# Kernel tuning notes

Hardware: AMD Instinct MI355X
Metric: run time of the kernel (lower is better)

## Reference

```python
import jax, jax.numpy as jnp
import numpy as np

E = 2048      # embedding_size
H = 16        # num_heads
D = 128       # head_dim
G = 4         # gqa_factor
KH = H // G   # kv heads
F = 8192      # up_proj_size
B, S = 2, 2048


def _layer_norm(x, g, b, eps=1e-5):
    mu = jnp.mean(x, axis=-1, keepdims=True)
    var = jnp.mean(jnp.square(x - mu), axis=-1, keepdims=True)
    return (x - mu) * jax.lax.rsqrt(var + eps) * g + b


def setup_inputs() -> dict:
    key = jax.random.key(0)
    ks = jax.random.split(key, 16)
    std = 0.02
    inp = {
        'x': jax.random.normal(ks[0], (B, S, E), dtype=jnp.float32),
        'ln1_g': jnp.ones((E,), jnp.float32),
        'ln1_b': jnp.zeros((E,), jnp.float32),
        'wq': jax.random.normal(ks[1], (E, H * D), jnp.float32) * std,
        'bq': jnp.zeros((H * D,), jnp.float32),
        'wk': jax.random.normal(ks[2], (E, KH * D), jnp.float32) * std,
        'bk': jnp.zeros((KH * D,), jnp.float32),
        'wv': jax.random.normal(ks[3], (E, KH * D), jnp.float32) * std,
        'bv': jnp.zeros((KH * D,), jnp.float32),
        'wo': jax.random.normal(ks[4], (H * D, E), jnp.float32) * std,
        'bo': jnp.zeros((E,), jnp.float32),
        'ln2_g': jnp.ones((E,), jnp.float32),
        'ln2_b': jnp.zeros((E,), jnp.float32),
        'wu': jax.random.normal(ks[5], (E, F), jnp.float32) * std,
        'bu': jnp.zeros((F,), jnp.float32),
        'wd': jax.random.normal(ks[6], (F, E), jnp.float32) * std,
        'bd': jnp.zeros((E,), jnp.float32),
    }
    return inp


def _block(x, ln1_g, ln1_b, wq, bq, wk, bk, wv, bv, wo, bo, ln2_g, ln2_b, wu, bu, wd, bd):
    b, s, e = x.shape
    # attention sub-block (use_cache=False, train_mode=False -> no dropout)
    x1 = _layer_norm(x, ln1_g, ln1_b)
    q = (x1 @ wq + bq).reshape(b, s, H, D).transpose(0, 2, 1, 3)       # (B,H,S,D)
    q = q.reshape(b, KH, G, s, D)                                       # (B,KH,G,S,D)
    k = (x1 @ wk + bk).reshape(b, s, KH, D).transpose(0, 2, 1, 3)      # (B,KH,S,D)
    v = (x1 @ wv + bv).reshape(b, s, KH, D).transpose(0, 2, 1, 3)      # (B,KH,S,D)
    scores = jnp.einsum('bkgsd,bktd->bkgst', q, k) / np.sqrt(D).astype(np.float32)
    causal = jnp.tril(jnp.ones((s, s), dtype=bool))                     # True = keep
    scores = jnp.where(causal, scores, -jnp.inf)
    att = jax.nn.softmax(scores, axis=-1)
    o = jnp.einsum('bkgst,bktd->bkgsd', att, v)                         # (B,KH,G,S,D)
    o = o.reshape(b, H, s, D).transpose(0, 2, 1, 3).reshape(b, s, H * D)
    x = x + (o @ wo + bo)
    # MLP sub-block
    x2 = _layer_norm(x, ln2_g, ln2_b)
    h = jax.nn.gelu(x2 @ wu + bu, approximate=False)
    x = x + (h @ wd + bd)
    return x


def reference(x, ln1_g, ln1_b, wq, bq, wk, bk, wv, bv, wo, bo, ln2_g, ln2_b, wu, bu, wd, bd):
    return _block(x, ln1_g, ln1_b, wq, bq, wk, bk, wv, bv, wo, bo, ln2_g, ln2_b, wu, bu, wd, bd)
```

## Files before the change

kernel.cpp:

```cpp
#include <hip/hip_runtime.h>
#include <hip/hip_bf16.h>
#include <cstdint>
#include <math.h>

typedef unsigned short u16;
using f32x4   = __attribute__((ext_vector_type(4))) float;
using short8  = __attribute__((ext_vector_type(8))) short;
using short4v = __attribute__((ext_vector_type(4))) short;

#define DEV static __device__ __forceinline__

DEV u16 f2bf(float f) {
  union { float f; unsigned u; } v; v.f = f;
  unsigned r = v.u + 0x7fffu + ((v.u >> 16) & 1u);
  return (u16)(r >> 16);
}

DEV f32x4 mfma_bf16(short8 a, short8 b, f32x4 c) {
  return __builtin_amdgcn_mfma_f32_16x16x32_bf16(a, b, c, 0, 0, 0);
}

DEV void gload16(const void* g, void* l) {
  __builtin_amdgcn_global_load_lds((const __attribute__((address_space(1))) void*)g,
                                   (__attribute__((address_space(3))) void*)l,
                                   16, 0, 0);
}

__global__ __launch_bounds__(256) void transpose_cvt(
    const float* __restrict__ in, u16* __restrict__ out, int K, int N)
{
  __shared__ float tile[32][33];
  const int n0 = blockIdx.x * 32, k0 = blockIdx.y * 32;
  const int c = threadIdx.x & 31, r = threadIdx.x >> 5;
#pragma unroll
  for (int i = 0; i < 4; i++) {
    const int row = r + i * 8;
    tile[row][c] = in[(size_t)(k0 + row) * N + n0 + c];
  }
  __syncthreads();
#pragma unroll
  for (int i = 0; i < 4; i++) {
    const int row = r + i * 8;
    out[(size_t)(n0 + row) * K + k0 + c] = f2bf(tile[c][row]);
  }
}

__global__ __launch_bounds__(256) void ln_kernel(
    const float* __restrict__ x, const float* __restrict__ g,
    const float* __restrict__ bt, u16* __restrict__ out)
{
  __shared__ float red1[4], red2[4];
  const int row = blockIdx.x;
  const int t = threadIdx.x;
  const int lane = t & 63, w = t >> 6;
  const float* xr = x + (size_t)row * 2048 + t * 8;
  float v[8];
  {
    const float4* p4 = (const float4*)xr;
    float4 a = p4[0], b = p4[1];
    v[0] = a.x; v[1] = a.y; v[2] = a.z; v[3] = a.w;
    v[4] = b.x; v[5] = b.y; v[6] = b.z; v[7] = b.w;
  }
  float s = 0.f;
#pragma unroll
  for (int j = 0; j < 8; j++) s += v[j];
#pragma unroll
  for (int m = 1; m < 64; m <<= 1) s += __shfl_xor(s, m);
  if (lane == 0) red1[w] = s;
  __syncthreads();
  const float mu = (red1[0] + red1[1] + red1[2] + red1[3]) * (1.f / 2048.f);
  float q = 0.f;
#pragma unroll
  for (int j = 0; j < 8; j++) { v[j] -= mu; q += v[j] * v[j]; }
#pragma unroll
  for (int m = 1; m < 64; m <<= 1) q += __shfl_xor(q, m);
  if (lane == 0) red2[w] = q;
  __syncthreads();
  const float rstd = rsqrtf((red2[0] + red2[1] + red2[2] + red2[3]) * (1.f / 2048.f) + 1e-5f);
  const float4* g4 = (const float4*)(g + t * 8);
  const float4* b4 = (const float4*)(bt + t * 8);
  float4 ga = g4[0], gb = g4[1], ba = b4[0], bb = b4[1];
  float gg[8] = {ga.x, ga.y, ga.z, ga.w, gb.x, gb.y, gb.z, gb.w};
  float bbv[8] = {ba.x, ba.y, ba.z, ba.w, bb.x, bb.y, bb.z, bb.w};
  short8 o;
#pragma unroll
  for (int j = 0; j < 8; j++) o[j] = (short)f2bf(v[j] * rstd * gg[j] + bbv[j]);
  *(short8*)&out[(size_t)row * 2048 + t * 8] = o;
}

template<int MODE, int N, int K>
__global__ void __launch_bounds__(256) gemm_bt(
    const u16* __restrict__ A, const u16* __restrict__ Bt,
    const float* __restrict__ bias,
    u16* __restrict__ out_bf)
{
  __shared__ u16 As[128 * 64];
  __shared__ u16 Bs[128 * 64];
  const int m0 = blockIdx.y * 128;
  const int n0 = blockIdx.x * 128;
  const int tid = threadIdx.x;
  const int lane = tid & 63, w = tid >> 6;
  const int wm = w >> 1, wn = w & 1;
  const int z = lane >> 4, l15 = lane & 15;

  f32x4 acc[4][4];
#pragma unroll
  for (int m = 0; m < 4; m++)
#pragma unroll
    for (int n = 0; n < 4; n++)
#pragma unroll
      for (int i = 0; i < 4; i++) acc[m][n][i] = 0.f;

  for (int k0 = 0; k0 < K; k0 += 64) {
#pragma unroll
    for (int j = 0; j < 4; j++) {
      const int seg = w * 4 + j;
      const int c = seg * 64 + lane;
      const int r = c >> 3;
      const int cc = (c & 7) ^ (r & 7);
      gload16(A + (size_t)(m0 + r) * K + k0 + cc * 8, &As[seg * 512]);
    }
#pragma unroll
    for (int j = 0; j < 4; j++) {
      const int seg = w * 4 + j;
      const int c = seg * 64 + lane;
      const int r = c >> 3;
      const int cc = (c & 7) ^ (r & 7);
      gload16(Bt + (size_t)(n0 + r) * K + k0 + cc * 8, &Bs[seg * 512]);
    }
    asm volatile("s_waitcnt vmcnt(0)" ::: "memory");
    __syncthreads();

#pragma unroll
    for (int kk = 0; kk < 2; kk++) {
      short8 af[4], bfr[4];
#pragma unroll
      for (int m = 0; m < 4; m++) {
        const int row = wm * 64 + m * 16 + l15;
        const int off = row * 64 + ((kk * 32 + z * 8) ^ ((row & 7) << 3));
        af[m] = *(const short8*)&As[off];
      }
#pragma unroll
      for (int n = 0; n < 4; n++) {
        const int row = wn * 64 + n * 16 + l15;
        const int off = row * 64 + ((kk * 32 + z * 8) ^ ((row & 7) << 3));
        bfr[n] = *(const short8*)&Bs[off];
      }
#pragma unroll
      for (int m = 0; m < 4; m++)
#pragma unroll
        for (int n = 0; n < 4; n++)
          acc[m][n] = mfma_bf16(af[m], bfr[n], acc[m][n]);
    }
    __syncthreads();
  }

#pragma unroll
  for (int m = 0; m < 4; m++) {
    const int row0 = m0 + wm * 64 + m * 16 + z * 4;
#pragma unroll
    for (int n = 0; n < 4; n++) {
      const int col = n0 + wn * 64 + n * 16 + l15;
      f32x4 v = acc[m][n];
      const float bb = bias[col];
      if constexpr (MODE == 1) {
#pragma unroll
        for (int i = 0; i < 4; i++)
          out_bf[(size_t)(row0 + i) * N + col] = f2bf(v[i] + bb);
      } else {
        const int bidx = row0 >> 11, sidx = row0 & 2047;
        const int kh = col >> 7, d = col & 127;
        short4v p;
#pragma unroll
        for (int i = 0; i < 4; i++) p[i] = (short)f2bf(v[i] + bb);
        *(short4v*)&out_bf[(size_t)((bidx * 4 + kh) * 128 + d) * 2048 + sidx] = p;
      }
    }
  }
}

template<int MODE, int BM, int N, int K>
__global__ void __launch_bounds__(512) gemm256(
    const u16* __restrict__ A, const u16* __restrict__ Bt,
    const float* __restrict__ bias, const float* __restrict__ resid,
    u16* __restrict__ out_bf, float* __restrict__ out_f)
{
  constexpr int BN = 256;
  constexpr int MREP = BM / 32;
  constexpr int LA = BM / 128;
  constexpr int P = K / 32;
  constexpr int NWG = (4096 / BM) * (N / BN);
  constexpr int CPX = NWG / 8;

  __shared__ u16 Al[4][BM * 32];
  __shared__ u16 Bl[4][BN * 32];

  const int bid = blockIdx.x;
  const int wg = (bid & 7) * CPX + (bid >> 3);
  const int bm = wg / (N / BN), bn = wg % (N / BN);
  const int m0 = bm * BM, n0 = bn * BN;
  const int tid = threadIdx.x, lane = tid & 63, w = tid >> 6;
  const int wm = w >> 2, wn = w & 3;
  const int z = lane >> 4, l15 = lane & 15;
  const int wmBase = wm * (BM / 2);
  const int wnBase = wn * 64;
  const int koff = (z ^ ((l15 >> 1) & 3)) * 8;
  const int col8 = ((lane & 3) ^ ((lane >> 3) & 3)) * 8;
  const int srow = lane >> 2;

  f32x4 acc[MREP][4];
#pragma unroll
  for (int m = 0; m < MREP; m++)
#pragma unroll
    for (int n = 0; n < 4; n++)
#pragma unroll
      for (int i = 0; i < 4; i++) acc[m][n][i] = 0.f;

  auto stage = [&](int g) {
    const int sl = g & 3;
    const int kc = g * 32;
#pragma unroll
    for (int j = 0; j < LA; j++) {
      const int sweep = w * LA + j;
      gload16(A + (size_t)(m0 + sweep * 16 + srow) * K + kc + col8, &Al[sl][sweep * 512]);
    }
#pragma unroll
    for (int j = 0; j < 2; j++) {
      const int sweep = w * 2 + j;
      gload16(Bt + (size_t)(n0 + sweep * 16 + srow) * K + kc + col8, &Bl[sl][sweep * 512]);
    }
  };

#define PHASE(pp, VMSTR, DOSTAGE)                                              \
  do {                                                                         \
    asm volatile("s_waitcnt " VMSTR ::: "memory");                             \
    __builtin_amdgcn_s_barrier();                                              \
    asm volatile("" ::: "memory");                                             \
    if (DOSTAGE) stage((pp) + 3);                                              \
    const int sl_ = (pp) & 3;                                                  \
    const u16* Ab_ = &Al[sl_][0];                                              \
    const u16* Bb_ = &Bl[sl_][0];                                              \
    short8 af_[MREP], bf_[4];                                                  \
    _Pragma("unroll")                                                          \
    for (int m = 0; m < MREP; m++)                                             \
      af_[m] = *(const short8*)&Ab_[(wmBase + m * 16 + l15) * 32 + koff];      \
    _Pragma("unroll")                                                          \
    for (int n = 0; n < 4; n++)                                                \
      bf_[n] = *(const short8*)&Bb_[(wnBase + n * 16 + l15) * 32 + koff];      \
    asm volatile("s_waitcnt lgkmcnt(0)" ::: "memory");                         \
    __builtin_amdgcn_sched_barrier(0);                                         \
    __builtin_amdgcn_s_setprio(1);                                             \
    _Pragma("unroll")                                                          \
    for (int m = 0; m < MREP; m++)                                             \
      _Pragma("unroll")                                                        \
      for (int n = 0; n < 4; n++)                                              \
        acc[m][n] = mfma_bf16(af_[m], bf_[n], acc[m][n]);                      \
    __builtin_amdgcn_s_setprio(0);                                             \
    asm volatile("" ::: "memory");                                             \
    __builtin_amdgcn_s_barrier();                                              \
  } while (0)

  stage(0); stage(1); stage(2);

  if constexpr (LA == 2) {
    for (int p = 0; p < P - 3; p++) PHASE(p, "vmcnt(8)", true);
    PHASE(P - 3, "vmcnt(8)", false);
    PHASE(P - 2, "vmcnt(4)", false);
    PHASE(P - 1, "vmcnt(0)", false);
  } else {
    for (int p = 0; p < P - 3; p++) PHASE(p, "vmcnt(6)", true);
    PHASE(P - 3, "vmcnt(6)", false);
    PHASE(P - 2, "vmcnt(3)", false);
    PHASE(P - 1, "vmcnt(0)", false);
  }
#undef PHASE

#pragma unroll
  for (int m = 0; m < MREP; m++) {
    const int row0 = m0 + wmBase + m * 16 + z * 4;
#pragma unroll
    for (int n = 0; n < 4; n++) {
      const int col = n0 + wnBase + n * 16 + l15;
      f32x4 v = acc[m][n];
      const float bb = bias[col];
      if constexpr (MODE == 0) {
#pragma unroll
        for (int i = 0; i < 4; i++)
          out_bf[(size_t)(row0 + i) * N + col] = f2bf((v[i] + bb) * 0.08838834764831845f);
      } else if constexpr (MODE == 3) {
#pragma unroll
        for (int i = 0; i < 4; i++) {
          const size_t idx = (size_t)(row0 + i) * N + col;
          out_f[idx] = v[i] + bb + resid[idx];
        }
      } else if constexpr (MODE == 4) {
#pragma unroll
        for (int i = 0; i < 4; i++) {
          const float xx = v[i] + bb;
          out_bf[(size_t)(row0 + i) * N + col] =
              f2bf(0.5f * xx * (1.f + erff(xx * 0.70710678118654752f)));
        }
      } else {
#pragma unroll
        for (int i = 0; i < 4; i++) {
          const size_t idx = (size_t)(row0 + i) * N + col;
          out_f[idx] = v[i] + bb + out_f[idx];
        }
      }
    }
  }
}

__global__ void __launch_bounds__(256) attn_kernel(
    const u16* __restrict__ qb, const u16* __restrict__ kb,
    const u16* __restrict__ vt, u16* __restrict__ ob)
{
  __shared__ u16 Kt[2][64 * 128];
  __shared__ u16 Vs[2][128 * 64];
  __shared__ u16 Pl[4 * 32 * 64];

  const int idx = blockIdx.x;
  const int xcd = idx & 7;
  const int u = (idx >> 3) & 31;
  const int half = idx >> 8;
  const int bh = xcd * 4 + (u & 3);
  const int qh = u >> 2;
  const int qt = half ? (15 - qh) : qh;

  const int b = bh >> 4, h = bh & 15, kh = h >> 2;
  const int q0 = qt * 128;
  const int tid = threadIdx.x, lane = tid & 63, w = tid >> 6;
  const int z = lane >> 4, l15 = lane & 15;
  const int qw0 = q0 + w * 32;
  const int ksw = (l15 & 7) << 3;

  short8 qf[2][4];
#pragma unroll
  for (int m = 0; m < 2; m++)
#pragma unroll
    for (int kk = 0; kk < 4; kk++)
      qf[m][kk] = *(const short8*)&qb[(size_t)(b * 2048 + qw0 + m * 16 + l15) * 2048 +
                                      h * 128 + kk * 32 + z * 8];

  f32x4 oacc[2][8];
#pragma unroll
  for (int m = 0; m < 2; m++)
#pragma unroll
    for (int n = 0; n < 8; n++)
#pragma unroll
      for (int i = 0; i < 4; i++) oacc[m][n][i] = 0.f;
  float mst[2][4], lst[2][4];
#pragma unroll
  for (int m = 0; m < 2; m++)
#pragma unroll
    for (int i = 0; i < 4; i++) { mst[m][i] = -1e30f; lst[m][i] = 0.f; }

  auto STAGE = [&](int tt, int bufsel) {
    const int kv0s = tt * 64;
#pragma unroll
    for (int j = 0; j < 4; j++) {
      const int seg = w * 4 + j;
      const int c = seg * 64 + lane;
      const int r = c >> 4;
      const int cc = (c & 15) ^ (r & 7);
      gload16(kb + (size_t)(b * 2048 + kv0s + r) * 512 + kh * 128 + cc * 8,
              &Kt[bufsel][seg * 512]);
    }
#pragma unroll
    for (int j = 0; j < 4; j++) {
      const int seg = w * 4 + j;
      const int c = seg * 64 + lane;
      const int d = c >> 3;
      const int cc = (c & 7) ^ (d & 7);
      gload16(vt + (size_t)((b * 4 + kh) * 128 + d) * 2048 + kv0s + cc * 8,
              &Vs[bufsel][seg * 512]);
    }
  };

  const int ntiles = q0 / 64 + 2;

  STAGE(0, 0);
  asm volatile("s_waitcnt vmcnt(0)" ::: "memory");
  __syncthreads();

  for (int t = 0; t < ntiles; t++) {
    const int cur = t & 1;
    if (t + 1 < ntiles) STAGE(t + 1, cur ^ 1);

    const int kv0 = t * 64;
    if (kv0 <= qw0 + 31) {
      f32x4 sf[2][4];
#pragma unroll
      for (int m = 0; m < 2; m++)
#pragma unroll
        for (int n = 0; n < 4; n++)
#pragma unroll
          for (int i = 0; i < 4; i++) sf[m][n][i] = 0.f;

      __builtin_amdgcn_s_setprio(1);
#pragma unroll
      for (int kk = 0; kk < 4; kk++) {
        short8 kfr[4];
#pragma unroll
        for (int n = 0; n < 4; n++) {
          const int row = n * 16 + l15;
          kfr[n] = *(const short8*)&Kt[cur][row * 128 + ((kk * 32 + z * 8) ^ ksw)];
        }
#pragma unroll
        for (int m = 0; m < 2; m++)
#pragma unroll
          for (int n = 0; n < 4; n++)
            sf[m][n] = mfma_bf16(qf[m][kk], kfr[n], sf[m][n]);
      }
      __builtin_amdgcn_s_setprio(0);

      u16* Pw = &Pl[w * 2048];
      const bool edge = (kv0 + 63 > qw0);
#pragma unroll
      for (int m = 0; m < 2; m++) {
#pragma unroll
        for (int i = 0; i < 4; i++) {
          const int rq = qw0 + m * 16 + z * 4 + i;
          if (edge) {
#pragma unroll
            for (int n = 0; n < 4; n++)
              if (kv0 + n * 16 + l15 > rq) sf[m][n][i] = -1e30f;
          }
          float mx = fmaxf(fmaxf(sf[m][0][i], sf[m][1][i]), fmaxf(sf[m][2][i], sf[m][3][i]));
          mx = fmaxf(mx, __shfl_xor(mx, 1));
          mx = fmaxf(mx, __shfl_xor(mx, 2));
          mx = fmaxf(mx, __shfl_xor(mx, 4));
          mx = fmaxf(mx, __shfl_xor(mx, 8));
          const bool grow = mx > mst[m][i];
          const float mn = grow ? mx : mst[m][i];
          float rs = 0.f;
#pragma unroll
          for (int n = 0; n < 4; n++) {
            const float p = __expf(sf[m][n][i] - mn);
            sf[m][n][i] = p;
            rs += p;
          }
          rs += __shfl_xor(rs, 1);
          rs += __shfl_xor(rs, 2);
          rs += __shfl_xor(rs, 4);
          rs += __shfl_xor(rs, 8);
          if (grow) {
            const float al = __expf(mst[m][i] - mx);
            mst[m][i] = mx;
            lst[m][i] = lst[m][i] * al + rs;
#pragma unroll
            for (int n = 0; n < 8; n++) oacc[m][n][i] *= al;
          } else {
            lst[m][i] += rs;
          }
          const int prow = m * 16 + z * 4 + i;
          const int psw = ((z * 4 + i) & 7) << 3;
#pragma unroll
          for (int n = 0; n < 4; n++)
            Pw[prow * 64 + ((n * 16 + l15) ^ psw)] = f2bf(sf[m][n][i]);
        }
      }

      __builtin_amdgcn_s_setprio(1);
#pragma unroll
      for (int kk = 0; kk < 2; kk++) {
        short8 af[2], vf[8];
#pragma unroll
        for (int m = 0; m < 2; m++) {
          const int row = m * 16 + l15;
          af[m] = *(const short8*)&Pw[row * 64 + ((kk * 32 + z * 8) ^ ksw)];
        }
#pragma unroll
        for (int n = 0; n < 8; n++) {
          const int row = n * 16 + l15;
          vf[n] = *(const short8*)&Vs[cur][row * 64 + ((kk * 32 + z * 8) ^ ksw)];
        }
#pragma unroll
        for (int m = 0; m < 2; m++)
#pragma unroll
          for (int n = 0; n < 8; n++)
            oacc[m][n] = mfma_bf16(af[m], vf[n], oacc[m][n]);
      }
      __builtin_amdgcn_s_setprio(0);
    }

    asm volatile("s_waitcnt vmcnt(0)" ::: "memory");
    __syncthreads();
  }

#pragma unroll
  for (int m = 0; m < 2; m++)
#pragma unroll
    for (int i = 0; i < 4; i++) {
      const float inv = 1.0f / lst[m][i];
      const int rq = qw0 + m * 16 + z * 4 + i;
      u16* orow = &ob[(size_t)(b * 2048 + rq) * 2048 + h * 128];
#pragma unroll
      for (int n = 0; n < 8; n++)
        orow[n * 16 + l15] = f2bf(oacc[m][n][i] * inv);
    }
}

extern "C" void kernel_launch(void* const* d_in, const int* in_sizes, int n_in,
                              void* d_out, int out_size, void* d_ws, size_t ws_size,
                              hipStream_t stream) {
  (void)in_sizes; (void)n_in; (void)out_size; (void)ws_size;
  const float* x     = (const float*)d_in[0];
  const float* ln1_g = (const float*)d_in[1];
  const float* ln1_b = (const float*)d_in[2];
  const float* wq    = (const float*)d_in[3];
  const float* bq    = (const float*)d_in[4];
  const float* wk    = (const float*)d_in[5];
  const float* bk    = (const float*)d_in[6];
  const float* wv    = (const float*)d_in[7];
  const float* bv    = (const float*)d_in[8];
  const float* wo    = (const float*)d_in[9];
  const float* bo    = (const float*)d_in[10];
  const float* ln2_g = (const float*)d_in[11];
  const float* ln2_b = (const float*)d_in[12];
  const float* wu    = (const float*)d_in[13];
  const float* bu    = (const float*)d_in[14];
  const float* wd    = (const float*)d_in[15];
  const float* bd    = (const float*)d_in[16];
  float* out = (float*)d_out;

  char* p = (char*)d_ws;
  u16* wqT = (u16*)p; p += (size_t)2048 * 2048 * 2;
  u16* wkT = (u16*)p; p += (size_t)512 * 2048 * 2;
  u16* wvT = (u16*)p; p += (size_t)512 * 2048 * 2;
  u16* woT = (u16*)p; p += (size_t)2048 * 2048 * 2;
  u16* wuT = (u16*)p; p += (size_t)8192 * 2048 * 2;
  u16* wdT = (u16*)p; p += (size_t)2048 * 8192 * 2;
  u16* x1  = (u16*)p; p += (size_t)4096 * 2048 * 2;
  u16* qbuf= (u16*)p; p += (size_t)4096 * 2048 * 2;
  u16* kbuf= (u16*)p; p += (size_t)4096 * 512 * 2;
  u16* vtb = (u16*)p; p += (size_t)4096 * 512 * 2;
  u16* hb  = (u16*)p; p += (size_t)4096 * 8192 * 2;
  u16* ob  = x1;
  u16* x2  = qbuf;

  transpose_cvt<<<dim3(64, 64),  256, 0, stream>>>(wq, wqT, 2048, 2048);
  transpose_cvt<<<dim3(16, 64),  256, 0, stream>>>(wk, wkT, 2048, 512);
  transpose_cvt<<<dim3(16, 64),  256, 0, stream>>>(wv, wvT, 2048, 512);
  transpose_cvt<<<dim3(64, 64),  256, 0, stream>>>(wo, woT, 2048, 2048);
  transpose_cvt<<<dim3(256, 64), 256, 0, stream>>>(wu, wuT, 2048, 8192);
  transpose_cvt<<<dim3(64, 256), 256, 0, stream>>>(wd, wdT, 8192, 2048);

  ln_kernel<<<4096, 256, 0, stream>>>(x, ln1_g, ln1_b, x1);

  gemm256<0, 128, 2048, 2048><<<256, 512, 0, stream>>>(x1, wqT, bq, nullptr, qbuf, nullptr);
  gemm_bt<1, 512, 2048><<<dim3(4, 32), 256, 0, stream>>>(x1, wkT, bk, kbuf);
  gemm_bt<2, 512, 2048><<<dim3(4, 32), 256, 0, stream>>>(x1, wvT, bv, vtb);

  attn_kernel<<<512, 256, 0, stream>>>(qbuf, kbuf, vtb, ob);

  gemm256<3, 128, 2048, 2048><<<256, 512, 0, stream>>>(ob, woT, bo, x, nullptr, out);

  ln_kernel<<<4096, 256, 0, stream>>>(out, ln2_g, ln2_b, x2);

  gemm256<4, 256, 8192, 2048><<<512, 512, 0, stream>>>(x2, wuT, bu, nullptr, hb, nullptr);
  gemm256<5, 128, 2048, 8192><<<256, 512, 0, stream>>>(hb, wdT, bd, nullptr, nullptr, out);
}
```

Measured before the change: 867.1 us.

## Replace 512-thread large-tile GEMM with 256-thread 128x128 tile kernel

Swaps the 512-thread GEMM (128x256 or 256x256 tiles) for a 256-thread kernel with fixed 128x128 tiles and 4x4 MFMA fragments per wave. It adds an XCD-aware block mapping that optionally stripes N tiles per XCD, and drops the trailing barrier in each pipeline phase. The aim is more resident workgroups per CU, better L2 locality per XCD and less barrier overhead. The cost is lower arithmetic intensity per tile, so more global and LDS traffic per FLOP.

```diff
diff --git a/kernel.cpp b/kernel.cpp
--- a/kernel.cpp
+++ b/kernel.cpp
@@ -179,38 +179,37 @@
   }
 }
 
-template<int MODE, int BM, int N, int K>
-__global__ void __launch_bounds__(512) gemm256(
+template<int MODE, int N, int K, int STRIPE_N>
+__global__ void __launch_bounds__(256) gemm_pd(
     const u16* __restrict__ A, const u16* __restrict__ Bt,
     const float* __restrict__ bias, const float* __restrict__ resid,
     u16* __restrict__ out_bf, float* __restrict__ out_f)
 {
-  constexpr int BN = 256;
-  constexpr int MREP = BM / 32;
-  constexpr int LA = BM / 128;
-  constexpr int P = K / 32;
-  constexpr int NWG = (4096 / BM) * (N / BN);
-  constexpr int CPX = NWG / 8;
-
-  __shared__ u16 Al[4][BM * 32];
-  __shared__ u16 Bl[4][BN * 32];
+  constexpr int TN = N / 128;
+  constexpr int NT = K / 32;
+
+  __shared__ u16 Al[4][128 * 32];
+  __shared__ u16 Bl[4][128 * 32];
 
   const int bid = blockIdx.x;
-  const int wg = (bid & 7) * CPX + (bid >> 3);
-  const int bm = wg / (N / BN), bn = wg % (N / BN);
-  const int m0 = bm * BM, n0 = bn * BN;
-  const int tid = threadIdx.x, lane = tid & 63, w = tid >> 6;
-  const int wm = w >> 2, wn = w & 3;
+  const int xcd = bid & 7, wl = bid >> 3;
+  int m0, n0;
+  if constexpr (STRIPE_N) {
+    constexpr int NSTR = TN / 8;
+    n0 = (xcd * NSTR + (wl % NSTR)) * 128;
+    m0 = (wl / NSTR) * 128;
+  } else {
+    m0 = (xcd * 4 + (wl & 3)) * 128;
+    n0 = (wl >> 2) * 128;
+  }
+  const int tid = threadIdx.x;
+  const int lane = tid & 63, w = tid >> 6;
+  const int wm = w >> 1, wn = w & 1;
   const int z = lane >> 4, l15 = lane & 15;
-  const int wmBase = wm * (BM / 2);
-  const int wnBase = wn * 64;
-  const int koff = (z ^ ((l15 >> 1) & 3)) * 8;
-  const int col8 = ((lane & 3) ^ ((lane >> 3) & 3)) * 8;
-  const int srow = lane >> 2;
-
-  f32x4 acc[MREP][4];
-#pragma unroll
-  for (int m = 0; m < MREP; m++)
+
+  f32x4 acc[4][4];
+#pragma unroll
+  for (int m = 0; m < 4; m++)
 #pragma unroll
     for (int n = 0; n < 4; n++)
 #pragma unroll
@@ -220,67 +219,63 @@
     const int sl = g & 3;
     const int kc = g * 32;
 #pragma unroll
-    for (int j = 0; j < LA; j++) {
-      const int sweep = w * LA + j;
-      gload16(A + (size_t)(m0 + sweep * 16 + srow) * K + kc + col8, &Al[sl][sweep * 512]);
-    }
-#pragma unroll
-    for (int j = 0; j < 2; j++) {
-      const int sweep = w * 2 + j;
-      gload16(Bt + (size_t)(n0 + sweep * 16 + srow) * K + kc + col8, &Bl[sl][sweep * 512]);
+    for (int s = 0; s < 2; s++) {
+      const int c = s * 256 + tid;
+      const int r = c >> 2, q = c & 3;
+      const int cg = q ^ ((r >> 1) & 3);
+      gload16(A + (size_t)(m0 + r) * K + kc + cg * 8, &Al[sl][c * 8]);
+    }
+#pragma unroll
+    for (int s = 0; s < 2; s++) {
+      const int c = s * 256 + tid;
+      const int r = c >> 2, q = c & 3;
+      const int cg = q ^ ((r >> 1) & 3);
+      gload16(Bt + (size_t)(n0 + r) * K + kc + cg * 8, &Bl[sl][c * 8]);
     }
   };
 
-#define PHASE(pp, VMSTR, DOSTAGE)                                              \
+#define PHASE(tt, VMSTR, DOSTAGE)                                              \
   do {                                                                         \
     asm volatile("s_waitcnt " VMSTR ::: "memory");                             \
     __builtin_amdgcn_s_barrier();                                              \
-    asm volatile("" ::: "memory");                                             \
-    if (DOSTAGE) stage((pp) + 3);                                              \
-    const int sl_ = (pp) & 3;                                                  \
-    const u16* Ab_ = &Al[sl_][0];                                              \
-    const u16* Bb_ = &Bl[sl_][0];                                              \
-    short8 af_[MREP], bf_[4];                                                  \
+    if (DOSTAGE) stage((tt) + 3);                                              \
+    const int sl_ = (tt) & 3;                                                  \
+    short8 af_[4], bf_[4];                                                     \
     _Pragma("unroll")                                                          \
-    for (int m = 0; m < MREP; m++)                                             \
-      af_[m] = *(const short8*)&Ab_[(wmBase + m * 16 + l15) * 32 + koff];      \
+    for (int m = 0; m < 4; m++) {                                              \
+      const int row = wm * 64 + m * 16 + l15;                                  \
+      af_[m] = *(const short8*)&Al[sl_][row * 32 + ((z ^ ((row >> 1) & 3)) * 8)]; \
+    }                                                                          \
     _Pragma("unroll")                                                          \
-    for (int n = 0; n < 4; n++)                                                \
-      bf_[n] = *(const short8*)&Bb_[(wnBase + n * 16 + l15) * 32 + koff];      \
+    for (int n = 0; n < 4; n++) {                                              \
+      const int row = wn * 64 + n * 16 + l15;                                  \
+      bf_[n] = *(const short8*)&Bl[sl_][row * 32 + ((z ^ ((row >> 1) & 3)) * 8)]; \
+    }                                                                          \
     asm volatile("s_waitcnt lgkmcnt(0)" ::: "memory");                         \
     __builtin_amdgcn_sched_barrier(0);                                         \
     __builtin_amdgcn_s_setprio(1);                                             \
     _Pragma("unroll")                                                          \
-    for (int m = 0; m < MREP; m++)                                             \
+    for (int m = 0; m < 4; m++)                                                \
       _Pragma("unroll")                                                        \
       for (int n = 0; n < 4; n++)                                              \
         acc[m][n] = mfma_bf16(af_[m], bf_[n], acc[m][n]);                      \
     __builtin_amdgcn_s_setprio(0);                                             \
-    asm volatile("" ::: "memory");                                             \
-    __builtin_amdgcn_s_barrier();                                              \
   } while (0)
 
   stage(0); stage(1); stage(2);
 
-  if constexpr (LA == 2) {
-    for (int p = 0; p < P - 3; p++) PHASE(p, "vmcnt(8)", true);
-    PHASE(P - 3, "vmcnt(8)", false);
-    PHASE(P - 2, "vmcnt(4)", false);
-    PHASE(P - 1, "vmcnt(0)", false);
-  } else {
-    for (int p = 0; p < P - 3; p++) PHASE(p, "vmcnt(6)", true);
-    PHASE(P - 3, "vmcnt(6)", false);
-    PHASE(P - 2, "vmcnt(3)", false);
-    PHASE(P - 1, "vmcnt(0)", false);
-  }
+  for (int t = 0; t < NT - 3; t++) PHASE(t, "vmcnt(8)", true);
+  PHASE(NT - 3, "vmcnt(8)", false);
+  PHASE(NT - 2, "vmcnt(4)", false);
+  PHASE(NT - 1, "vmcnt(0)", false);
 #undef PHASE
 
 #pragma unroll
-  for (int m = 0; m < MREP; m++) {
-    const int row0 = m0 + wmBase + m * 16 + z * 4;
+  for (int m = 0; m < 4; m++) {
+    const int row0 = m0 + wm * 64 + m * 16 + z * 4;
 #pragma unroll
     for (int n = 0; n < 4; n++) {
-      const int col = n0 + wnBase + n * 16 + l15;
+      const int col = n0 + wn * 64 + n * 16 + l15;
       f32x4 v = acc[m][n];
       const float bb = bias[col];
       if constexpr (MODE == 0) {
@@ -548,16 +543,16 @@
 
   ln_kernel<<<4096, 256, 0, stream>>>(x, ln1_g, ln1_b, x1);
 
-  gemm256<0, 128, 2048, 2048><<<256, 512, 0, stream>>>(x1, wqT, bq, nullptr, qbuf, nullptr);
+  gemm_pd<0, 2048, 2048, 0><<<512, 256, 0, stream>>>(x1, wqT, bq, nullptr, qbuf, nullptr);
   gemm_bt<1, 512, 2048><<<dim3(4, 32), 256, 0, stream>>>(x1, wkT, bk, kbuf);
   gemm_bt<2, 512, 2048><<<dim3(4, 32), 256, 0, stream>>>(x1, wvT, bv, vtb);
 
   attn_kernel<<<512, 256, 0, stream>>>(qbuf, kbuf, vtb, ob);
 
-  gemm256<3, 128, 2048, 2048><<<256, 512, 0, stream>>>(ob, woT, bo, x, nullptr, out);
+  gemm_pd<3, 2048, 2048, 0><<<512, 256, 0, stream>>>(ob, woT, bo, x, nullptr, out);
 
   ln_kernel<<<4096, 256, 0, stream>>>(out, ln2_g, ln2_b, x2);
 
-  gemm256<4, 256, 8192, 2048><<<512, 512, 0, stream>>>(x2, wuT, bu, nullptr, hb, nullptr);
-  gemm256<5, 128, 2048, 8192><<<256, 512, 0, stream>>>(hb, wdT, bd, nullptr, nullptr, out);
-}
+  gemm_pd<4, 8192, 2048, 1><<<2048, 256, 0, stream>>>(x2, wuT, bu, nullptr, hb, nullptr);
+  gemm_pd<5, 2048, 8192, 1><<<512, 256, 0, stream>>>(hb, wdT, bd, nullptr, nullptr, out);
+}
```

New measurement: 825.6 us. 4.8% less time.
